# Performance work log

Measured on AMD Instinct MI355X. Metric: run time of the kernel, lower is better.

## Reference

```python
import jax, jax.numpy as jnp
import numpy as np

N_NODES = 50000
N_EDGES = 800000
N_GRAPHS = 2500
HIDDEN = 64
IN_DIM = 14  # 11 QM9 features + 3 pos


def setup_inputs() -> dict:
    key = jax.random.key(0)
    ks = jax.random.split(key, 12)
    def glorot(k, shape):
        fan_in = shape[0]
        return jax.random.normal(k, shape, dtype=jnp.float32) / np.sqrt(fan_in)
    return {
        "x": jax.random.normal(ks[0], (N_NODES, 11), dtype=jnp.float32),
        "pos": jax.random.normal(ks[1], (N_NODES, 3), dtype=jnp.float32),
        "edge_index": jax.random.randint(ks[2], (2, N_EDGES), 0, N_NODES, dtype=jnp.int64),
        "batch": jnp.sort(jax.random.randint(ks[3], (N_NODES,), 0, N_GRAPHS, dtype=jnp.int64)),
        "W1a": glorot(ks[4], (IN_DIM, HIDDEN)),
        "b1a": jnp.zeros((HIDDEN,), jnp.float32),
        "W1b": glorot(ks[5], (HIDDEN, HIDDEN)),
        "b1b": jnp.zeros((HIDDEN,), jnp.float32),
        "W2a": glorot(ks[6], (HIDDEN, HIDDEN)),
        "b2a": jnp.zeros((HIDDEN,), jnp.float32),
        "W2b": glorot(ks[7], (HIDDEN, HIDDEN)),
        "b2b": jnp.zeros((HIDDEN,), jnp.float32),
        "Wlin": glorot(ks[8], (HIDDEN, 1)),
        "blin": jnp.zeros((1,), jnp.float32),
    }


def reference(x, pos, edge_index, batch, W1a, b1a, W1b, b1b, W2a, b2a, W2b, b2b, Wlin, blin):
    n = x.shape[0]
    src, dst = edge_index[0], edge_index[1]

    def gin_conv(h, Wa, ba, Wb, bb):
        # GINConv (eps=0): nn((1+eps)*h + sum_{j in N(i)} h_j)
        agg = jax.ops.segment_sum(h[src], dst, num_segments=n)  # scatter-add over edges
        z = h + agg
        return jax.nn.relu(z @ Wa + ba) @ Wb + bb

    h = jnp.concatenate([x, pos], axis=1)  # [N, 14]
    h = jax.nn.relu(gin_conv(h, W1a, b1a, W1b, b1b))
    h = jax.nn.relu(gin_conv(h, W2a, b2a, W2b, b2b))

    # global_mean_pool over graph ids
    sums = jax.ops.segment_sum(h, batch, num_segments=N_GRAPHS)            # [G, H]
    counts = jax.ops.segment_sum(jnp.ones((n,), h.dtype), batch, num_segments=N_GRAPHS)
    pooled = sums / jnp.maximum(counts, 1.0)[:, None]
    return pooled @ Wlin + blin  # [G, 1]
```

## Files before the change

### kernel.cpp

```cpp
#include <hip/hip_runtime.h>
#include <hip/hip_fp16.h>


typedef unsigned int uint;
typedef _Float16 half8 __attribute__((ext_vector_type(8)));
typedef float f32x4 __attribute__((ext_vector_type(4)));

#define BSH   6
#define NBKMAX 1024
#define EPB   4096
#define CAPSH 11
#define CAP   (1 << CAPSH)
#define ZBLK  64

__device__ __forceinline__ void addu(float* a, uint d) {
    __half2 h = *(__half2*)&d;
    a[0] += __low2float(h);
    a[1] += __high2float(h);
}
__device__ __forceinline__ half8 as_half8(uint4 u) {
    union { uint4 u; half8 h; } x; x.u = u; return x.h;
}


__global__ __launch_bounds__(256) void pack_bin(
    const float* __restrict__ x, const float* __restrict__ pos,
    uint2* __restrict__ xp2,
    const int* __restrict__ src, const int* __restrict__ dst,
    int* __restrict__ bkt_cnt, uint* __restrict__ pairs,
    const float* __restrict__ W1a, const float* __restrict__ W1b,
    const float* __restrict__ W2a, const float* __restrict__ W2b,
    _Float16* __restrict__ wp1a, _Float16* __restrict__ wp1b,
    _Float16* __restrict__ wp2a, _Float16* __restrict__ wp2b,
    uint4* __restrict__ zbuf, int nz4,
    int packb, int nbk, int N, int E)
{
    int bx = (int)blockIdx.x;
    if (bx < ZBLK) {
        uint4 z4 = {0u, 0u, 0u, 0u};
        for (int idx = bx * 256 + threadIdx.x; idx < nz4; idx += ZBLK * 256)
            zbuf[idx] = z4;
        return;
    }
    bx -= ZBLK;
    if (bx == 0) {
        for (int idx = threadIdx.x; idx < 64 * 32; idx += 256) {
            int n = idx >> 5, k = idx & 31;
            wp1a[idx] = (k < 14) ? (_Float16)W1a[k * 64 + n] : (_Float16)0.f;
        }
        for (int idx = threadIdx.x; idx < 64 * 64; idx += 256) {
            int n = idx >> 6, k = idx & 63;
            wp1b[idx] = (_Float16)W1b[k * 64 + n];
            wp2a[idx] = (_Float16)W2a[k * 64 + n];
            wp2b[idx] = (_Float16)W2b[k * 64 + n];
        }
        return;
    }
    bx -= 1;
    if (bx < packb) {
        int i = bx * 256 + threadIdx.x;
        if (i >= N) return;
        float v[16];
#pragma unroll
        for (int k = 0; k < 11; k++) v[k] = x[(size_t)i * 11 + k];
        v[11] = pos[(size_t)i * 3 + 0];
        v[12] = pos[(size_t)i * 3 + 1];
        v[13] = pos[(size_t)i * 3 + 2];
        v[14] = 0.f; v[15] = 0.f;
#pragma unroll
        for (int c = 0; c < 4; c++) {
            __half2 l = __floats2half2_rn(v[4 * c],     v[4 * c + 1]);
            __half2 h = __floats2half2_rn(v[4 * c + 2], v[4 * c + 3]);
            uint2 u;
            u.x = *(uint*)&l;
            u.y = *(uint*)&h;
            xp2[(size_t)i * 4 + c] = u;
        }
        return;
    }
    bx -= packb;
    __shared__ int lcnt[NBKMAX];
    __shared__ int lbase[NBKMAX];
    for (int i = threadIdx.x; i < nbk; i += 256) lcnt[i] = 0;
    __syncthreads();
    int e0 = bx * EPB + threadIdx.x;
    uint pv[EPB / 256];
    int  rk[EPB / 256], bk[EPB / 256];
#pragma unroll
    for (int j = 0; j < EPB / 256; j++) {
        int e = e0 + j * 256;
        bk[j] = -1;
        if (e < E) {
            int s = src[e];
            int d = dst[e];
            bk[j] = d >> BSH;
            pv[j] = ((uint)(d & ((1 << BSH) - 1)) << 16) | (uint)s;
            rk[j] = atomicAdd(&lcnt[bk[j]], 1);
        }
    }
    __syncthreads();
    for (int i = threadIdx.x; i < nbk; i += 256) {
        int c = lcnt[i];
        lbase[i] = c ? atomicAdd(&bkt_cnt[i], c) : 0;
    }
    __syncthreads();
#pragma unroll
    for (int j = 0; j < EPB / 256; j++) {
        if (bk[j] >= 0) {
            int p = lbase[bk[j]] + rk[j];
            if (p < CAP)
                pairs[((size_t)bk[j] << CAPSH) + p] = pv[j];
        }
    }
}


__global__ __launch_bounds__(256) void bucket_build(
    const uint* __restrict__ pairs, const int* __restrict__ bkt_cnt,
    int* __restrict__ offs, int* __restrict__ deg,
    int* __restrict__ ssrc, int N)
{
    __shared__ int cnt[256];
    __shared__ int cur[256];
    __shared__ int wsum[4];
    int b = blockIdx.x;
    int nbase = b << BSH;
    int nn = min(1 << BSH, N - nbase);
    cnt[threadIdx.x] = 0;
    __syncthreads();
    int start = b << CAPSH;
    int end = start + min(bkt_cnt[b], CAP);
    for (int e = start + threadIdx.x; e < end; e += 256)
        atomicAdd(&cnt[pairs[e] >> 16], 1);
    __syncthreads();
    int v = cnt[threadIdx.x];
    int lane = threadIdx.x & 63, w = threadIdx.x >> 6;
    int s = v;
#pragma unroll
    for (int off2 = 1; off2 < 64; off2 <<= 1) {
        int t = __shfl_up(s, off2, 64);
        if (lane >= off2) s += t;
    }
    if (lane == 63) wsum[w] = s;
    __syncthreads();
    int add = 0;
    for (int j = 0; j < w; j++) add += wsum[j];
    int gofs = start + (s + add - v);
    if (threadIdx.x < nn) {
        offs[nbase + threadIdx.x] = gofs;
        deg[nbase + threadIdx.x]  = v;
    }
    cur[threadIdx.x] = gofs;
    __syncthreads();
    for (int e = start + threadIdx.x; e < end; e += 256) {
        uint pr = pairs[e];
        int p = atomicAdd(&cur[pr >> 16], 1);
        ssrc[p] = (int)(pr & 0xffffu);
    }
}


__global__ __launch_bounds__(256) void gather1_mlp1(
    const uint2* __restrict__ xp2,
    const int* __restrict__ offs, const int* __restrict__ deg,
    const int* __restrict__ ssrc,
    const _Float16* __restrict__ wp1a, const _Float16* __restrict__ wp1b,
    const float* __restrict__ b1a, const float* __restrict__ b1b,
    uint* __restrict__ h1p)
{
    __shared__ uint4 zb[16 * 2];
    __shared__ float hb[16 * 68];
    int lane = threadIdx.x & 63;
    int wid  = threadIdx.x >> 6;
    int i0 = blockIdx.x << 4;
    int n0 = i0 + wid * 4;

    int stv = 0, lnv = 0;
    if (lane < 4) { stv = offs[n0 + lane]; lnv = deg[n0 + lane]; }
    int n  = lane >> 4;
    int s  = (lane >> 2) & 3;
    int c  = lane & 3;
    int dn = __shfl(lnv, n, 64);
    int st = __shfl(stv, n, 64);
    int pA = lane & 15;
    int svA = 0, svB = 0;
    if (dn > 0)  svA = ssrc[st + min(pA, dn - 1)];
    if (dn > 16) svB = ssrc[st + min(16 + pA, dn - 1)];
    uint2 S = {0u, 0u};
    if (s == 0) S = xp2[(size_t)(n0 + n) * 4 + c];

    float a[4] = {0.f, 0.f, 0.f, 0.f};
#pragma unroll
    for (int it = 0; it < 4; ++it) {
        int pos = it * 4 + s;
        int sA = __shfl(svA, (n << 4) | pos, 64);
        if (pos < dn) {
            uint2 A = xp2[(size_t)sA * 4 + c];
            addu(a + 0, A.x); addu(a + 2, A.y);
        }
    }
    if (__any(dn > 16)) {
#pragma unroll
        for (int it = 4; it < 8; ++it) {
            int pos = it * 4 + s;
            int sB = __shfl(svB, (n << 4) | (pos - 16), 64);
            if (pos < dn) {
                uint2 A = xp2[(size_t)sB * 4 + c];
                addu(a + 0, A.x); addu(a + 2, A.y);
            }
        }
        int pos2 = 32 + s;
        while (__any(pos2 < dn)) {
            if (pos2 < dn) {
                int sid = ssrc[st + pos2];
                uint2 A = xp2[(size_t)sid * 4 + c];
                addu(a + 0, A.x); addu(a + 2, A.y);
            }
            pos2 += 4;
        }
    }
#pragma unroll
    for (int mm = 4; mm <= 8; mm <<= 1)
#pragma unroll
        for (int d = 0; d < 4; d++) a[d] += __shfl_xor(a[d], mm, 64);
    if (s == 0) {
        addu(a + 0, S.x); addu(a + 2, S.y);
        __half2 l  = __floats2half2_rn(a[0], a[1]);
        __half2 hh = __floats2half2_rn(a[2], a[3]);
        uint2 u;
        u.x = *(uint*)&l;
        u.y = *(uint*)&hh;
        ((uint2*)zb)[(wid * 4 + n) * 4 + c] = u;
    }
    __syncthreads();

    int m = lane & 15, quad = lane >> 4;
    int half = lane >> 5, p = lane & 31;
    int nw = wid * 16 + m;
    half8 BA  = *(const half8*)(wp1a + (size_t)nw * 32 + quad * 8);
    half8 BB0 = *(const half8*)(wp1b + (size_t)nw * 64 + quad * 8);
    half8 BB1 = *(const half8*)(wp1b + (size_t)nw * 64 + 32 + quad * 8);
    float baw = b1a[nw], bbw = b1b[nw];

    half8 A0;
#pragma unroll
    for (int jj = 0; jj < 8; jj++) A0[jj] = (_Float16)0.f;
    if (quad < 2)
        A0 = as_half8(zb[m * 2 + quad]);
    f32x4 acc = (f32x4){baw, baw, baw, baw};
    acc = __builtin_amdgcn_mfma_f32_16x16x32_f16(A0, BA, acc, 0, 0, 0);
#pragma unroll
    for (int r = 0; r < 4; r++)
        hb[(quad * 4 + r) * 68 + wid * 16 + m] = fmaxf(acc[r], 0.f);
    __syncthreads();
    half8 A1[2];
#pragma unroll
    for (int hh = 0; hh < 2; hh++)
#pragma unroll
        for (int jj = 0; jj < 8; jj++)
            A1[hh][jj] = (_Float16)hb[m * 68 + hh * 32 + quad * 8 + jj];
    f32x4 acc2 = (f32x4){bbw, bbw, bbw, bbw};
    acc2 = __builtin_amdgcn_mfma_f32_16x16x32_f16(A1[0], BB0, acc2, 0, 0, 0);
    acc2 = __builtin_amdgcn_mfma_f32_16x16x32_f16(A1[1], BB1, acc2, 0, 0, 0);
    __syncthreads();
#pragma unroll
    for (int r = 0; r < 4; r++)
        hb[(quad * 4 + r) * 68 + wid * 16 + m] = fmaxf(acc2[r], 0.f);
    __syncthreads();
#pragma unroll
    for (int it = 0; it < 2; it++) {
        int row = wid * 4 + it * 2 + half;
        float lo = hb[row * 68 + 2 * p];
        float hi = hb[row * 68 + 2 * p + 1];
        __half2 hh2 = __floats2half2_rn(lo, hi);
        h1p[(size_t)(i0 + row) * 32 + p] = *(uint*)&hh2;
    }
}


__global__ __launch_bounds__(256) void gather2_mlp2pool(
    const uint4* __restrict__ h4,
    const int* __restrict__ offs, const int* __restrict__ deg,
    const int* __restrict__ ssrc,
    const _Float16* __restrict__ wp2a, const _Float16* __restrict__ wp2b,
    const float* __restrict__ b2a, const float* __restrict__ b2b,
    const int* __restrict__ batch,
    float* __restrict__ sums, float* __restrict__ counts)
{
    __shared__ uint4 zb[16 * 8];
    __shared__ float hb[16 * 68];
    int lane = threadIdx.x & 63;
    int wid  = threadIdx.x >> 6;
    int i0 = blockIdx.x << 4;
    int n0 = i0 + wid * 4;

    int stv = 0, lnv = 0;
    if (lane < 4) { stv = offs[n0 + lane]; lnv = deg[n0 + lane]; }
    int n  = lane >> 4;
    int s  = (lane >> 3) & 1;
    int q  = lane & 7;
    int dn = __shfl(lnv, n, 64);
    int st = __shfl(stv, n, 64);
    int pA = lane & 15;
    int svA = 0, svB = 0;
    if (dn > 0)  svA = ssrc[st + min(pA, dn - 1)];
    if (dn > 16) svB = ssrc[st + min(16 + pA, dn - 1)];
    uint4 S = {0u, 0u, 0u, 0u};
    if (s == 0) S = h4[(size_t)(n0 + n) * 8 + q];

    float a[8] = {0.f, 0.f, 0.f, 0.f, 0.f, 0.f, 0.f, 0.f};
#pragma unroll
    for (int it = 0; it < 8; ++it) {
        int pos = it * 2 + s;
        int sA = __shfl(svA, (n << 4) | pos, 64);
        if (pos < dn) {
            uint4 A = h4[(size_t)sA * 8 + q];
            addu(a + 0, A.x); addu(a + 2, A.y); addu(a + 4, A.z); addu(a + 6, A.w);
        }
    }
    if (__any(dn > 16)) {
#pragma unroll
        for (int it = 8; it < 16; ++it) {
            int pos = it * 2 + s;
            int sB = __shfl(svB, (n << 4) | (pos - 16), 64);
            if (pos < dn) {
                uint4 A = h4[(size_t)sB * 8 + q];
                addu(a + 0, A.x); addu(a + 2, A.y); addu(a + 4, A.z); addu(a + 6, A.w);
            }
        }
        int pos2 = 32 + s;
        while (__any(pos2 < dn)) {
            if (pos2 < dn) {
                int sid = ssrc[st + pos2];
                uint4 A = h4[(size_t)sid * 8 + q];
                addu(a + 0, A.x); addu(a + 2, A.y); addu(a + 4, A.z); addu(a + 6, A.w);
            }
            pos2 += 2;
        }
    }
#pragma unroll
    for (int d = 0; d < 8; d++) a[d] += __shfl_xor(a[d], 8, 64);
    if (s == 0) {
        addu(a + 0, S.x); addu(a + 2, S.y); addu(a + 4, S.z); addu(a + 6, S.w);
        __half2 p0 = __floats2half2_rn(a[0], a[1]);
        __half2 p1 = __floats2half2_rn(a[2], a[3]);
        __half2 p2 = __floats2half2_rn(a[4], a[5]);
        __half2 p3 = __floats2half2_rn(a[6], a[7]);
        uint4 o4;
        o4.x = *(uint*)&p0; o4.y = *(uint*)&p1;
        o4.z = *(uint*)&p2; o4.w = *(uint*)&p3;
        zb[(wid * 4 + n) * 8 + q] = o4;
    }
    __syncthreads();

    int m = lane & 15, quad = lane >> 4;
    int nw = wid * 16 + m;
    half8 BA0 = *(const half8*)(wp2a + (size_t)nw * 64 + quad * 8);
    half8 BA1 = *(const half8*)(wp2a + (size_t)nw * 64 + 32 + quad * 8);
    half8 BB0 = *(const half8*)(wp2b + (size_t)nw * 64 + quad * 8);
    half8 BB1 = *(const half8*)(wp2b + (size_t)nw * 64 + 32 + quad * 8);
    float baw = b2a[nw], bbw = b2b[nw];

    half8 A0[2];
#pragma unroll
    for (int hh = 0; hh < 2; hh++)
        A0[hh] = as_half8(zb[m * 8 + hh * 4 + quad]);
    f32x4 acc = (f32x4){baw, baw, baw, baw};
    acc = __builtin_amdgcn_mfma_f32_16x16x32_f16(A0[0], BA0, acc, 0, 0, 0);
    acc = __builtin_amdgcn_mfma_f32_16x16x32_f16(A0[1], BA1, acc, 0, 0, 0);
#pragma unroll
    for (int r = 0; r < 4; r++)
        hb[(quad * 4 + r) * 68 + wid * 16 + m] = fmaxf(acc[r], 0.f);
    __syncthreads();
    half8 A1[2];
#pragma unroll
    for (int hh = 0; hh < 2; hh++)
#pragma unroll
        for (int jj = 0; jj < 8; jj++)
            A1[hh][jj] = (_Float16)hb[m * 68 + hh * 32 + quad * 8 + jj];
    f32x4 acc2 = (f32x4){bbw, bbw, bbw, bbw};
    acc2 = __builtin_amdgcn_mfma_f32_16x16x32_f16(A1[0], BB0, acc2, 0, 0, 0);
    acc2 = __builtin_amdgcn_mfma_f32_16x16x32_f16(A1[1], BB1, acc2, 0, 0, 0);
    __syncthreads();
#pragma unroll
    for (int r = 0; r < 4; r++)
        hb[(quad * 4 + r) * 68 + wid * 16 + m] = fmaxf(acc2[r], 0.f);
    __syncthreads();

    int gcur = batch[i0 + wid * 4]; float ps = 0.f; int cntn = 0;
#pragma unroll
    for (int nn = 0; nn < 4; nn++) {
        int row = wid * 4 + nn;
        float v = hb[row * 68 + lane];
        int gi = batch[i0 + row];
        if (gi != gcur) {
            atomicAdd(&sums[gcur * 64 + lane], ps);
            if (lane == 0) atomicAdd(&counts[gcur], (float)cntn);
            gcur = gi; ps = 0.f; cntn = 0;
        }
        ps += v; cntn++;
    }
    atomicAdd(&sums[gcur * 64 + lane], ps);
    if (lane == 0) atomicAdd(&counts[gcur], (float)cntn);
}

__global__ __launch_bounds__(256) void gin_final(
    const float* __restrict__ sums, const float* __restrict__ counts,
    const float* __restrict__ Wlin, const float* __restrict__ blin,
    float* __restrict__ out, int G)
{
    int lane = threadIdx.x & 63;
    int g    = blockIdx.x * 4 + (threadIdx.x >> 6);
    if (g < G) {
        float v = sums[g * 64 + lane] * Wlin[lane];
#pragma unroll
        for (int off = 32; off > 0; off >>= 1) v += __shfl_down(v, off, 64);
        if (lane == 0) out[g] = v / fmaxf(counts[g], 1.0f) + blin[0];
    }
}

extern "C" void kernel_launch(void* const* d_in, const int* in_sizes, int n_in,
                              void* d_out, int out_size, void* d_ws, size_t ws_size,
                              hipStream_t stream) {
    const float* x    = (const float*)d_in[0];
    const float* pos  = (const float*)d_in[1];
    const int*   ei   = (const int*)d_in[2];
    const int*   batch= (const int*)d_in[3];
    const float* W1a  = (const float*)d_in[4];
    const float* b1a  = (const float*)d_in[5];
    const float* W1b  = (const float*)d_in[6];
    const float* b1b  = (const float*)d_in[7];
    const float* W2a  = (const float*)d_in[8];
    const float* b2a  = (const float*)d_in[9];
    const float* W2b  = (const float*)d_in[10];
    const float* b2b  = (const float*)d_in[11];
    const float* Wlin = (const float*)d_in[12];
    const float* blin = (const float*)d_in[13];
    float* out = (float*)d_out;

    const int N = in_sizes[0] / 11;
    const int E = in_sizes[2] / 2;
    const int G = out_size;

    const int* src = ei;
    const int* dst = ei + E;
    const int nbk   = (N + (1 << BSH) - 1) >> BSH;
    const int packb = (N + 255) / 256;
    const int neb   = (E + EPB - 1) / EPB;
    const int NG    = N >> 4;

    char* ws = (char*)d_ws;
    size_t o = 0;
    float* sums    = (float*)(ws + o); o += (size_t)G * 64 * 4;
    float* counts  = (float*)(ws + o); o += (((size_t)G + 63) & ~(size_t)63) * 4;
    const int nz4  = (int)(((size_t)G * 64 + (((size_t)G + 63) & ~(size_t)63)) / 4);
    int*   bkt_cnt = (int*)(ws + o);   o += NBKMAX * 4;
    o = (o + 255) & ~(size_t)255;
    _Float16* wp1a = (_Float16*)(ws + o); o += 64 * 32 * 2;
    o = (o + 255) & ~(size_t)255;
    _Float16* wp1b = (_Float16*)(ws + o); o += 64 * 64 * 2;
    o = (o + 255) & ~(size_t)255;
    _Float16* wp2a = (_Float16*)(ws + o); o += 64 * 64 * 2;
    o = (o + 255) & ~(size_t)255;
    _Float16* wp2b = (_Float16*)(ws + o); o += 64 * 64 * 2;
    o = (o + 255) & ~(size_t)255;
    int*   offs    = (int*)(ws + o);   o += (size_t)N * 4;
    int*   deg     = (int*)(ws + o);   o += (size_t)N * 4;
    o = (o + 255) & ~(size_t)255;
    int*   ssrc    = (int*)(ws + o);   o += ((size_t)nbk << CAPSH) * 4;
    o = (o + 255) & ~(size_t)255;
    uint*  h1p     = (uint*)(ws + o);  o += (size_t)N * 32 * 4;
    o = (o + 255) & ~(size_t)255;
    uint2* xp2     = (uint2*)(ws + o); o += (size_t)N * 32;
    o = (o + 255) & ~(size_t)255;
    uint*  pairs   = (uint*)(ws + o);  o += ((size_t)nbk << CAPSH) * 4;

    hipMemsetAsync(bkt_cnt, 0, NBKMAX * 4, stream);

    pack_bin<<<ZBLK + 1 + packb + neb, 256, 0, stream>>>(
        x, pos, xp2, src, dst, bkt_cnt, pairs,
        W1a, W1b, W2a, W2b, wp1a, wp1b, wp2a, wp2b,
        (uint4*)sums, nz4, packb, nbk, N, E);
    bucket_build<<<nbk, 256, 0, stream>>>(pairs, bkt_cnt, offs, deg, ssrc, N);
    gather1_mlp1<<<NG, 256, 0, stream>>>(
        xp2, offs, deg, ssrc, wp1a, wp1b, b1a, b1b, h1p);
    gather2_mlp2pool<<<NG, 256, 0, stream>>>(
        (const uint4*)h1p, offs, deg, ssrc, wp2a, wp2b, b2a, b2b,
        batch, sums, counts);
    gin_final<<<(G + 3) / 4, 256, 0, stream>>>(
        sums, counts, Wlin, blin, out, G);
}
```

Measured before the change: 147.8 us.

## Count node degrees with global atomics during binning and halve edges per block

```diff
diff --git a/kernel.cpp b/kernel.cpp
--- a/kernel.cpp
+++ b/kernel.cpp
@@ -8,7 +8,7 @@
 
 #define BSH   6
 #define NBKMAX 1024
-#define EPB   4096
+#define EPB   2048
 #define CAPSH 11
 #define CAP   (1 << CAPSH)
 #define ZBLK  64
@@ -27,7 +27,8 @@
     const float* __restrict__ x, const float* __restrict__ pos,
     uint2* __restrict__ xp2,
     const int* __restrict__ src, const int* __restrict__ dst,
-    int* __restrict__ bkt_cnt, uint* __restrict__ pairs,
+    int* __restrict__ bkt_cnt, int* __restrict__ deg,
+    uint* __restrict__ pairs,
     const float* __restrict__ W1a, const float* __restrict__ W1b,
     const float* __restrict__ W2a, const float* __restrict__ W2b,
     _Float16* __restrict__ wp1a, _Float16* __restrict__ wp1b,
@@ -96,6 +97,7 @@
             bk[j] = d >> BSH;
             pv[j] = ((uint)(d & ((1 << BSH) - 1)) << 16) | (uint)s;
             rk[j] = atomicAdd(&lcnt[bk[j]], 1);
+            atomicAdd(&deg[d], 1);
         }
     }
     __syncthreads();
@@ -117,42 +119,30 @@
 
 __global__ __launch_bounds__(256) void bucket_build(
     const uint* __restrict__ pairs, const int* __restrict__ bkt_cnt,
-    int* __restrict__ offs, int* __restrict__ deg,
-    int* __restrict__ ssrc, int N)
+    const int* __restrict__ deg,
+    int* __restrict__ offs, int* __restrict__ ssrc, int N)
 {
-    __shared__ int cnt[256];
-    __shared__ int cur[256];
-    __shared__ int wsum[4];
+    __shared__ int cur[64];
     int b = blockIdx.x;
     int nbase = b << BSH;
     int nn = min(1 << BSH, N - nbase);
-    cnt[threadIdx.x] = 0;
-    __syncthreads();
+    int tid = threadIdx.x;
     int start = b << CAPSH;
+    if (tid < 64) {
+        int v = (tid < nn) ? deg[nbase + tid] : 0;
+        int s = v;
+#pragma unroll
+        for (int off2 = 1; off2 < 64; off2 <<= 1) {
+            int t = __shfl_up(s, off2, 64);
+            if (tid >= off2) s += t;
+        }
+        int gofs = start + s - v;
+        if (tid < nn) offs[nbase + tid] = gofs;
+        cur[tid] = gofs;
+    }
+    __syncthreads();
     int end = start + min(bkt_cnt[b], CAP);
-    for (int e = start + threadIdx.x; e < end; e += 256)
-        atomicAdd(&cnt[pairs[e] >> 16], 1);
-    __syncthreads();
-    int v = cnt[threadIdx.x];
-    int lane = threadIdx.x & 63, w = threadIdx.x >> 6;
-    int s = v;
-#pragma unroll
-    for (int off2 = 1; off2 < 64; off2 <<= 1) {
-        int t = __shfl_up(s, off2, 64);
-        if (lane >= off2) s += t;
-    }
-    if (lane == 63) wsum[w] = s;
-    __syncthreads();
-    int add = 0;
-    for (int j = 0; j < w; j++) add += wsum[j];
-    int gofs = start + (s + add - v);
-    if (threadIdx.x < nn) {
-        offs[nbase + threadIdx.x] = gofs;
-        deg[nbase + threadIdx.x]  = v;
-    }
-    cur[threadIdx.x] = gofs;
-    __syncthreads();
-    for (int e = start + threadIdx.x; e < end; e += 256) {
+    for (int e = start + tid; e < end; e += 256) {
         uint pr = pairs[e];
         int p = atomicAdd(&cur[pr >> 16], 1);
         ssrc[p] = (int)(pr & 0xffffu);
@@ -455,6 +445,7 @@
     float* counts  = (float*)(ws + o); o += (((size_t)G + 63) & ~(size_t)63) * 4;
     const int nz4  = (int)(((size_t)G * 64 + (((size_t)G + 63) & ~(size_t)63)) / 4);
     int*   bkt_cnt = (int*)(ws + o);   o += NBKMAX * 4;
+    int*   deg     = (int*)(ws + o);   o += (size_t)N * 4;
     o = (o + 255) & ~(size_t)255;
     _Float16* wp1a = (_Float16*)(ws + o); o += 64 * 32 * 2;
     o = (o + 255) & ~(size_t)255;
@@ -465,7 +456,6 @@
     _Float16* wp2b = (_Float16*)(ws + o); o += 64 * 64 * 2;
     o = (o + 255) & ~(size_t)255;
     int*   offs    = (int*)(ws + o);   o += (size_t)N * 4;
-    int*   deg     = (int*)(ws + o);   o += (size_t)N * 4;
     o = (o + 255) & ~(size_t)255;
     int*   ssrc    = (int*)(ws + o);   o += ((size_t)nbk << CAPSH) * 4;
     o = (o + 255) & ~(size_t)255;
@@ -475,13 +465,13 @@
     o = (o + 255) & ~(size_t)255;
     uint*  pairs   = (uint*)(ws + o);  o += ((size_t)nbk << CAPSH) * 4;
 
-    hipMemsetAsync(bkt_cnt, 0, NBKMAX * 4, stream);
+    hipMemsetAsync(bkt_cnt, 0, NBKMAX * 4 + (size_t)N * 4, stream);
 
     pack_bin<<<ZBLK + 1 + packb + neb, 256, 0, stream>>>(
-        x, pos, xp2, src, dst, bkt_cnt, pairs,
+        x, pos, xp2, src, dst, bkt_cnt, deg, pairs,
         W1a, W1b, W2a, W2b, wp1a, wp1b, wp2a, wp2b,
         (uint4*)sums, nz4, packb, nbk, N, E);
-    bucket_build<<<nbk, 256, 0, stream>>>(pairs, bkt_cnt, offs, deg, ssrc, N);
+    bucket_build<<<nbk, 256, 0, stream>>>(pairs, bkt_cnt, deg, offs, ssrc, N);
     gather1_mlp1<<<NG, 256, 0, stream>>>(
         xp2, offs, deg, ssrc, wp1a, wp1b, b1a, b1b, h1p);
     gather2_mlp2pool<<<NG, 256, 0, stream>>>(
```

New measurement: 180.9 us. 1.22x slower.

## Stage binned edges in shared memory for coalesced bucket writes, widen buckets

Applied to the files above, without the earlier changes.

```diff
diff --git a/kernel.cpp b/kernel.cpp
--- a/kernel.cpp
+++ b/kernel.cpp
@@ -6,10 +6,10 @@
 typedef _Float16 half8 __attribute__((ext_vector_type(8)));
 typedef float f32x4 __attribute__((ext_vector_type(4)));
 
-#define BSH   6
-#define NBKMAX 1024
-#define EPB   4096
-#define CAPSH 11
+#define BSH   7
+#define NBKMAX 512
+#define EPB   2048
+#define CAPSH 12
 #define CAP   (1 << CAPSH)
 #define ZBLK  64
 
@@ -79,11 +79,15 @@
         return;
     }
     bx -= packb;
-    __shared__ int lcnt[NBKMAX];
-    __shared__ int lbase[NBKMAX];
-    for (int i = threadIdx.x; i < nbk; i += 256) lcnt[i] = 0;
-    __syncthreads();
-    int e0 = bx * EPB + threadIdx.x;
+    __shared__ int  lcnt[NBKMAX];
+    __shared__ int  lgofs[NBKMAX];
+    __shared__ uint spv[EPB];
+    __shared__ int  wsum2[4];
+    __shared__ int  ltot;
+    int tid = threadIdx.x;
+    lcnt[2 * tid] = 0; lcnt[2 * tid + 1] = 0;
+    __syncthreads();
+    int e0 = bx * EPB + tid;
     uint pv[EPB / 256];
     int  rk[EPB / 256], bk[EPB / 256];
 #pragma unroll
@@ -94,23 +98,45 @@
             int s = src[e];
             int d = dst[e];
             bk[j] = d >> BSH;
-            pv[j] = ((uint)(d & ((1 << BSH) - 1)) << 16) | (uint)s;
+            pv[j] = ((uint)d << 16) | (uint)s;
             rk[j] = atomicAdd(&lcnt[bk[j]], 1);
         }
     }
     __syncthreads();
-    for (int i = threadIdx.x; i < nbk; i += 256) {
-        int c = lcnt[i];
-        lbase[i] = c ? atomicAdd(&bkt_cnt[i], c) : 0;
-    }
-    __syncthreads();
-#pragma unroll
-    for (int j = 0; j < EPB / 256; j++) {
-        if (bk[j] >= 0) {
-            int p = lbase[bk[j]] + rk[j];
-            if (p < CAP)
-                pairs[((size_t)bk[j] << CAPSH) + p] = pv[j];
-        }
+    int v0 = lcnt[2 * tid], v1 = lcnt[2 * tid + 1];
+    int sum = v0 + v1;
+    int lane = tid & 63, w = tid >> 6;
+    int s = sum;
+#pragma unroll
+    for (int off2 = 1; off2 < 64; off2 <<= 1) {
+        int t = __shfl_up(s, off2, 64);
+        if (lane >= off2) s += t;
+    }
+    if (lane == 63) wsum2[w] = s;
+    __syncthreads();
+    int add = 0;
+    for (int j = 0; j < w; j++) add += wsum2[j];
+    int excl = s - sum + add;
+    int lb0 = excl, lb1 = excl + v0;
+    int g0b = v0 ? atomicAdd(&bkt_cnt[2 * tid], v0) : 0;
+    int g1b = v1 ? atomicAdd(&bkt_cnt[2 * tid + 1], v1) : 0;
+    lgofs[2 * tid]     = ((2 * tid) << CAPSH) + g0b - lb0;
+    lgofs[2 * tid + 1] = ((2 * tid + 1) << CAPSH) + g1b - lb1;
+    lcnt[2 * tid] = lb0; lcnt[2 * tid + 1] = lb1;
+    if (tid == 255) ltot = excl + sum;
+    __syncthreads();
+#pragma unroll
+    for (int j = 0; j < EPB / 256; j++)
+        if (bk[j] >= 0)
+            spv[lcnt[bk[j]] + rk[j]] = pv[j];
+    __syncthreads();
+    int tot = ltot;
+    for (int p = tid; p < tot; p += 256) {
+        uint v = spv[p];
+        int b = (int)(v >> 16) >> BSH;
+        int addr = lgofs[b] + p;
+        if ((addr >> CAPSH) == b)
+            pairs[addr] = v;
     }
 }
 
@@ -120,21 +146,22 @@
     int* __restrict__ offs, int* __restrict__ deg,
     int* __restrict__ ssrc, int N)
 {
-    __shared__ int cnt[256];
-    __shared__ int cur[256];
+    __shared__ int cnt[1 << BSH];
+    __shared__ int cur[1 << BSH];
     __shared__ int wsum[4];
     int b = blockIdx.x;
     int nbase = b << BSH;
     int nn = min(1 << BSH, N - nbase);
-    cnt[threadIdx.x] = 0;
+    int tid = threadIdx.x;
+    if (tid < (1 << BSH)) cnt[tid] = 0;
     __syncthreads();
     int start = b << CAPSH;
     int end = start + min(bkt_cnt[b], CAP);
-    for (int e = start + threadIdx.x; e < end; e += 256)
-        atomicAdd(&cnt[pairs[e] >> 16], 1);
-    __syncthreads();
-    int v = cnt[threadIdx.x];
-    int lane = threadIdx.x & 63, w = threadIdx.x >> 6;
+    for (int e = start + tid; e < end; e += 256)
+        atomicAdd(&cnt[(pairs[e] >> 16) & ((1 << BSH) - 1)], 1);
+    __syncthreads();
+    int v = (tid < (1 << BSH)) ? cnt[tid] : 0;
+    int lane = tid & 63, w = tid >> 6;
     int s = v;
 #pragma unroll
     for (int off2 = 1; off2 < 64; off2 <<= 1) {
@@ -146,15 +173,15 @@
     int add = 0;
     for (int j = 0; j < w; j++) add += wsum[j];
     int gofs = start + (s + add - v);
-    if (threadIdx.x < nn) {
-        offs[nbase + threadIdx.x] = gofs;
-        deg[nbase + threadIdx.x]  = v;
-    }
-    cur[threadIdx.x] = gofs;
-    __syncthreads();
-    for (int e = start + threadIdx.x; e < end; e += 256) {
+    if (tid < nn) {
+        offs[nbase + tid] = gofs;
+        deg[nbase + tid]  = v;
+    }
+    if (tid < (1 << BSH)) cur[tid] = gofs;
+    __syncthreads();
+    for (int e = start + tid; e < end; e += 256) {
         uint pr = pairs[e];
-        int p = atomicAdd(&cur[pr >> 16], 1);
+        int p = atomicAdd(&cur[(pr >> 16) & ((1 << BSH) - 1)], 1);
         ssrc[p] = (int)(pr & 0xffffu);
     }
 }
```

New measurement: 158.6 us. +7.3%, slower.
